# Optimization experiments

Hardware: AMD Instinct MI355X
Metric: run time of the kernel (lower is better)

Reference implementation:

```python
import jax, jax.numpy as jnp
import numpy as np
from jax import lax

P = 10  # patch_size


def _conv(x, w, b, pad):
    y = lax.conv_general_dilated(x, w, (1, 1), [(pad, pad), (pad, pad)],
                                 dimension_numbers=('NCHW', 'OIHW', 'NCHW'))
    return y + b[None, :, None, None]


def setup_inputs() -> dict:
    key = jax.random.key(0)
    ks = jax.random.split(key, 9)
    B, Cin, H, W = 8, 3, 320, 320
    classes = 2
    p2 = P * P
    s = 0.05
    return {
        'x': jax.random.normal(ks[0], (B, Cin, H, W), jnp.float32),
        'w_conv1': jax.random.normal(ks[1], (64, Cin, 7, 7), jnp.float32) * s,
        'b_conv1': jax.random.normal(ks[2], (64,), jnp.float32) * s,
        'w_conv2': jax.random.normal(ks[3], (classes, 64, 3, 3), jnp.float32) * s,
        'b_conv2': jax.random.normal(ks[4], (classes,), jnp.float32) * s,
        'w_fm': jax.random.normal(ks[5], (classes, Cin, 1, 1), jnp.float32) * s,
        'b_fm': jax.random.normal(ks[6], (classes,), jnp.float32) * s,
        'w_lin1': jax.random.normal(ks[7], (2 * p2, p2), jnp.float32) * s,  # torch Linear [out,in]
        'w_lin2': jax.random.normal(ks[8], (p2, 2 * p2), jnp.float32) * s,
    }


def reference(x, w_conv1, b_conv1, w_conv2, b_conv2, w_fm, b_fm, w_lin1, w_lin2):
    p = P
    ini = _conv(_conv(x, w_conv1, b_conv1, 3), w_conv2, b_conv2, 1)  # [B,classes,H,W]
    fea = _conv(x, w_fm, b_fm, 0) / 4.0                              # [B,classes,H,W]
    B, C, H, W = ini.shape
    L = (H // p) * (W // p)

    def unfold(t):  # non-overlapping patches: [B,C,H,W] -> [B,C,L,p*p]
        t = t.reshape(B, C, H // p, p, W // p, p)
        return t.transpose(0, 1, 2, 4, 3, 5).reshape(B, C, L, p * p)

    def trans(t):  # Linear(p2->2p2) -> Linear(2p2->p2) -> ReLU, per patch
        h = jnp.einsum('bclp,qp->bclq', t, w_lin1)
        return jax.nn.relu(jnp.einsum('bclq,pq->bclp', h, w_lin2))

    ui = trans(unfold(ini))   # [B,C,L,p2]
    uf = trans(unfold(fea))   # [B,C,L,p2]
    att = jnp.einsum('bclp,bcmp->bclm', ui, uf) / (p * p)  # [B,C,L,L]
    return att
```

## Files before the change

kernel.cpp:

```cpp
#include <hip/hip_runtime.h>

#define WS_M      0
#define WS_K      10000
#define WS_BETA   12646
#define WS_W9     12664
#define WS_BT     13150
#define WS_UIT    (16384 + 1638400)
#define WS_UFT    (16384 + 2*1638400)

typedef short bf16x8 __attribute__((ext_vector_type(8)));
typedef float f32x4  __attribute__((ext_vector_type(4)));

__device__ inline ushort f2bf(float f) {
    unsigned u = __float_as_uint(f);
    unsigned r = (u + 0x7fffu + ((u >> 16) & 1u)) >> 16;
    return (ushort)r;
}

__global__ __launch_bounds__(256) void k_prep(const float* __restrict__ wl1,
                                              const float* __restrict__ wl2,
                                              const float* __restrict__ wc1,
                                              const float* __restrict__ bc1,
                                              const float* __restrict__ wc2,
                                              const float* __restrict__ bc2,
                                              float* __restrict__ ws) {
    int blk = blockIdx.x;
    int t = threadIdx.x;
    if (blk < 40) {
        int idx = blk * 256 + t;
        if (idx < 10000) {
            int p = idx / 100, r = idx % 100;
            float s = 0.f;
            for (int q = 0; q < 200; ++q)
                s += wl2[p * 200 + q] * wl1[q * 100 + r];
            ws[WS_M + r * 100 + p] = s;
        }
        return;
    }
    __shared__ float swc1[9408];
    __shared__ float swc2[1152];
    __shared__ float sBeta[18];
    for (int i = t; i < 9408; i += 256) swc1[i] = wc1[i];
    for (int i = t; i < 1152; i += 256) swc2[i] = wc2[i];
    __syncthreads();
    if (blk < 43) {
        int base = (blk - 40) * 882;
        for (int ii = t; ii < 882; ii += 256) {
            int idx = base + ii;
            int v = idx % 7; int t1 = idx / 7;
            int u = t1 % 7;  int t2 = t1 / 7;
            int ci = t2 % 3; int t3 = t2 / 3;
            int b = t3 % 3;  int t4 = t3 / 3;
            int a = t4 % 3;  int c = t4 / 3;
            float s = 0.f;
            for (int c64 = 0; c64 < 64; ++c64)
                s += swc2[((c * 64 + c64) * 3 + a) * 3 + b] *
                     swc1[((c64 * 3 + ci) * 7 + u) * 7 + v];
            ws[WS_K + idx] = s;
        }
        if (blk == 40) {
            if (t < 18) {
                int b = t % 3; int a = (t / 3) % 3; int c = t / 9;
                float s = 0.f;
                for (int c64 = 0; c64 < 64; ++c64)
                    s += swc2[((c * 64 + c64) * 3 + a) * 3 + b] * bc1[c64];
                sBeta[t] = s; ws[WS_BETA + t] = s;
            }
            __syncthreads();
            if (t < 2) {
                float s = bc2[t];
                for (int j2 = 0; j2 < 9; ++j2) s += sBeta[t * 9 + j2];
                ws[WS_BT + t] = s;
            }
        }
    } else {
        int idx = (blk - 43) * 243 + t;
        if (t < 243) {
            int dx = idx % 9; int t1 = idx / 9;
            int dy = t1 % 9;  int t2 = t1 / 9;
            int ci = t2 % 3;  int c = t2 / 3;
            float s = 0.f;
            for (int a = 0; a < 3; ++a) {
                int u = dy - a; if (u < 0 || u > 6) continue;
                for (int b = 0; b < 3; ++b) {
                    int v = dx - b; if (v < 0 || v > 6) continue;
                    for (int c64 = 0; c64 < 64; ++c64)
                        s += swc2[((c * 64 + c64) * 3 + a) * 3 + b] *
                             swc1[((c64 * 3 + ci) * 7 + u) * 7 + v];
                }
            }
            ws[WS_W9 + idx] = s;
        }
    }
}

__global__ __launch_bounds__(256, 6) void k_fuse(const float* __restrict__ x,
                                                 const float* __restrict__ wfm,
                                                 const float* __restrict__ bfm,
                                                 const float* __restrict__ ws,
                                                 ushort* __restrict__ uiL,
                                                 ushort* __restrict__ ufL) {
    __shared__ float sx[3][28][36];
    __shared__ float sP[2][100][8];
    const int bx = blockIdx.x, by = blockIdx.y, b = blockIdx.z;
    const int t = threadIdx.x;
    const float* Mt   = ws + WS_M;
    const float* Kw   = ws + WS_K;
    const float* Beta = ws + WS_BETA;
    const float* W9   = ws + WS_W9;
    const float* Bt   = ws + WS_BT;
    const int gh0 = by * 20, gw0 = bx * 20;

    for (int idx = t; idx < 3 * 28 * 28; idx += 256) {
        int ci = idx / 784; int rem = idx - ci * 784;
        int rr = rem / 28, cc = rem - rr * 28;
        int gh = gh0 - 4 + rr, gw = gw0 - 4 + cc;
        float v = 0.f;
        if ((unsigned)gh < 320u && (unsigned)gw < 320u)
            v = x[(b * 3 + ci) * 102400 + gh * 320 + gw];
        sx[ci][rr][cc] = v;
    }
    __syncthreads();

    const int lh = t / 10, lw0 = (t % 10) * 2;
    if (t < 200) {
        float acc0[2], acc1[2];
        float bt0 = Bt[0], bt1 = Bt[1];
        acc0[0] = bt0; acc0[1] = bt0; acc1[0] = bt1; acc1[1] = bt1;
        #pragma unroll
        for (int ci = 0; ci < 3; ++ci) {
            #pragma unroll
            for (int dy = 0; dy < 9; ++dy) {
                const float* xr = &sx[ci][lh + dy][lw0];
                float2 y0 = *(const float2*)(xr);
                float2 y1 = *(const float2*)(xr + 2);
                float2 y2 = *(const float2*)(xr + 4);
                float2 y3 = *(const float2*)(xr + 6);
                float2 y4 = *(const float2*)(xr + 8);
                float xv[10] = {y0.x, y0.y, y1.x, y1.y, y2.x,
                                y2.y, y3.x, y3.y, y4.x, y4.y};
                #pragma unroll
                for (int dx = 0; dx < 9; ++dx) {
                    float w0t = W9[ci * 81 + dy * 9 + dx];
                    float w1t = W9[243 + ci * 81 + dy * 9 + dx];
                    acc0[0] += w0t * xv[dx];
                    acc0[1] += w0t * xv[dx + 1];
                    acc1[0] += w1t * xv[dx];
                    acc1[1] += w1t * xv[dx + 1];
                }
            }
        }
        #pragma unroll
        for (int j = 0; j < 2; ++j) {
            int lw = lw0 + j;
            int li = (lh / 10) * 2 + lw / 10;
            int r  = (lh % 10) * 10 + lw % 10;
            sP[0][r][li] = acc0[j];
            sP[1][r][li] = acc1[j];
        }
    }
    __syncthreads();

    bool edgeblk = (by == 0) | (by == 15) | (bx == 0) | (bx == 15);
    if (edgeblk) {
        for (int e = t; e < 400; e += 256) {
            int elh = e / 20, elw = e % 20;
            int h = gh0 + elh, w = gw0 + elw;
            if (h == 0 || h == 319 || w == 0 || w == 319) {
                float c0 = 0.f, c1 = 0.f;
                for (int a = 0; a < 3; ++a) {
                    int hh = h + a - 1;
                    for (int bb = 0; bb < 3; ++bb) {
                        int wwp = w + bb - 1;
                        bool invalid = ((unsigned)hh >= 320u) | ((unsigned)wwp >= 320u);
                        if (invalid) {
                            c0 += Beta[a * 3 + bb];
                            c1 += Beta[9 + a * 3 + bb];
                            for (int ci = 0; ci < 3; ++ci) {
                                const float* Kc = Kw + ((a * 3 + bb) * 3 + ci) * 49;
                                #pragma unroll
                                for (int u = 0; u < 7; ++u) {
                                    #pragma unroll
                                    for (int v = 0; v < 7; ++v) {
                                        float xv = sx[ci][elh + a + u][elw + bb + v];
                                        c0 += Kc[u * 7 + v] * xv;
                                        c1 += Kc[1323 + u * 7 + v] * xv;
                                    }
                                }
                            }
                        }
                    }
                }
                int li = (elh / 10) * 2 + elw / 10;
                int r  = (elh % 10) * 10 + elw % 10;
                sP[0][r][li] -= c0;
                sP[1][r][li] -= c1;
            }
        }
    }
    __syncthreads();

    auto trans = [&](ushort* outL) {
        if (t < 200) {
            int plane = (t >= 100) ? 1 : 0;
            int p = t - plane * 100;
            int bc = b * 2 + plane;
            float acc[4] = {0.f, 0.f, 0.f, 0.f};
            for (int r = 0; r < 100; ++r) {
                float m = Mt[r * 100 + p];
                f32x4 s = *(const f32x4*)&sP[plane][r][0];
                #pragma unroll
                for (int k = 0; k < 4; ++k) acc[k] += m * s[k];
            }
            #pragma unroll
            for (int k = 0; k < 4; ++k) {
                int l = (by * 2 + (k >> 1)) * 32 + bx * 2 + (k & 1);
                outL[((size_t)bc * 1024 + l) * 128 + p] = f2bf(fmaxf(acc[k], 0.f));
            }
        } else if (t < 256) {
            int task = t - 200;
            if (task < 56) {
                int plane = task / 28; int rem = task % 28;
                int k = rem / 7, q = rem % 7;
                int bc = b * 2 + plane;
                int l = (by * 2 + (k >> 1)) * 32 + bx * 2 + (k & 1);
                *(uint2*)&outL[((size_t)bc * 1024 + l) * 128 + 100 + q * 4] =
                    make_uint2(0u, 0u);
            }
        }
    };

    trans(uiL);
    __syncthreads();

    if (t < 200) {
        float wf00 = wfm[0], wf01 = wfm[1], wf02 = wfm[2];
        float wf10 = wfm[3], wf11 = wfm[4], wf12 = wfm[5];
        float bf0 = bfm[0], bf1 = bfm[1];
        #pragma unroll
        for (int j = 0; j < 2; ++j) {
            int lw = lw0 + j;
            float s0 = sx[0][4 + lh][4 + lw];
            float s1 = sx[1][4 + lh][4 + lw];
            float s2 = sx[2][4 + lh][4 + lw];
            float v0 = (bf0 + s0 * wf00 + s1 * wf01 + s2 * wf02) * 0.25f;
            float v1 = (bf1 + s0 * wf10 + s1 * wf11 + s2 * wf12) * 0.25f;
            int li = (lh / 10) * 2 + lw / 10;
            int r  = (lh % 10) * 10 + lw % 10;
            sP[0][r][li] = v0;
            sP[1][r][li] = v1;
        }
    }
    __syncthreads();

    trans(ufL);
}

__global__ __launch_bounds__(256) void k_att(const ushort* __restrict__ ui,
                                             const ushort* __restrict__ uf,
                                             float* __restrict__ out) {
    int bc   = blockIdx.z;
    int row0 = blockIdx.y * 128, col0 = blockIdx.x * 128;
    int wave = threadIdx.x >> 6, lane = threadIdx.x & 63;
    int r0 = row0 + (wave >> 1) * 64;
    int c0 = col0 + (wave & 1) * 64;
    int m = lane & 15, quad = lane >> 4;
    const ushort* ub = ui + (size_t)bc * 1024 * 128;
    const ushort* vb = uf + (size_t)bc * 1024 * 128;
    f32x4 acc[4][4];
    #pragma unroll
    for (int i = 0; i < 4; ++i)
        #pragma unroll
        for (int j = 0; j < 4; ++j)
            acc[i][j] = (f32x4){0.f, 0.f, 0.f, 0.f};
    #pragma unroll
    for (int k0 = 0; k0 < 128; k0 += 32) {
        bf16x8 af[4], bfr[4];
        #pragma unroll
        for (int i = 0; i < 4; ++i)
            af[i] = *(const bf16x8*)&ub[(size_t)(r0 + i * 16 + m) * 128 + k0 + quad * 8];
        #pragma unroll
        for (int j = 0; j < 4; ++j)
            bfr[j] = *(const bf16x8*)&vb[(size_t)(c0 + j * 16 + m) * 128 + k0 + quad * 8];
        #pragma unroll
        for (int i = 0; i < 4; ++i)
            #pragma unroll
            for (int j = 0; j < 4; ++j)
                acc[i][j] = __builtin_amdgcn_mfma_f32_16x16x32_bf16(af[i], bfr[j], acc[i][j], 0, 0, 0);
    }
    #pragma unroll
    for (int i = 0; i < 4; ++i) {
        #pragma unroll
        for (int r = 0; r < 4; ++r) {
            int row = r0 + i * 16 + quad * 4 + r;
            float* o = out + ((size_t)bc * 1024 + row) * 1024;
            #pragma unroll
            for (int j = 0; j < 4; ++j)
                o[c0 + j * 16 + m] = acc[i][j][r] * 0.01f;
        }
    }
}

extern "C" void kernel_launch(void* const* d_in, const int* in_sizes, int n_in,
                              void* d_out, int out_size, void* d_ws, size_t ws_size,
                              hipStream_t stream) {
    const float* x       = (const float*)d_in[0];
    const float* w_conv1 = (const float*)d_in[1];
    const float* b_conv1 = (const float*)d_in[2];
    const float* w_conv2 = (const float*)d_in[3];
    const float* b_conv2 = (const float*)d_in[4];
    const float* w_fm    = (const float*)d_in[5];
    const float* b_fm    = (const float*)d_in[6];
    const float* w_lin1  = (const float*)d_in[7];
    const float* w_lin2  = (const float*)d_in[8];
    float* out = (float*)d_out;
    float* ws  = (float*)d_ws;
    ushort* uiL = (ushort*)(ws + WS_UIT);
    ushort* ufL = (ushort*)(ws + WS_UFT);

    k_prep<<<45, 256, 0, stream>>>(w_lin1, w_lin2, w_conv1, b_conv1, w_conv2, b_conv2, ws);
    k_fuse<<<dim3(16, 16, 8), 256, 0, stream>>>(x, w_fm, b_fm, ws, uiL, ufL);
    k_att<<<dim3(8, 8, 16), 256, 0, stream>>>(uiL, ufL, out);
}
```

Measured before the change: 212.0 us.

## Stage patch outputs in shared memory for vector stores and shrink attention tiles

```diff
diff --git a/kernel.cpp b/kernel.cpp
--- a/kernel.cpp
+++ b/kernel.cpp
@@ -94,13 +94,17 @@
     }
 }
 
-__global__ __launch_bounds__(256, 6) void k_fuse(const float* __restrict__ x,
+__global__ __launch_bounds__(256, 8) void k_fuse(const float* __restrict__ x,
                                                  const float* __restrict__ wfm,
                                                  const float* __restrict__ bfm,
                                                  const float* __restrict__ ws,
                                                  ushort* __restrict__ uiL,
                                                  ushort* __restrict__ ufL) {
-    __shared__ float sx[3][28][36];
+    union alignas(16) SMemU {
+        float  sx[3][28][36];
+        ushort sOut[2][4][128];
+    };
+    __shared__ SMemU smu;
     __shared__ float sP[2][100][8];
     const int bx = blockIdx.x, by = blockIdx.y, b = blockIdx.z;
     const int t = threadIdx.x;
@@ -118,7 +122,7 @@
         float v = 0.f;
         if ((unsigned)gh < 320u && (unsigned)gw < 320u)
             v = x[(b * 3 + ci) * 102400 + gh * 320 + gw];
-        sx[ci][rr][cc] = v;
+        smu.sx[ci][rr][cc] = v;
     }
     __syncthreads();
 
@@ -131,7 +135,7 @@
         for (int ci = 0; ci < 3; ++ci) {
             #pragma unroll
             for (int dy = 0; dy < 9; ++dy) {
-                const float* xr = &sx[ci][lh + dy][lw0];
+                const float* xr = &smu.sx[ci][lh + dy][lw0];
                 float2 y0 = *(const float2*)(xr);
                 float2 y1 = *(const float2*)(xr + 2);
                 float2 y2 = *(const float2*)(xr + 4);
@@ -182,7 +186,7 @@
                                 for (int u = 0; u < 7; ++u) {
                                     #pragma unroll
                                     for (int v = 0; v < 7; ++v) {
-                                        float xv = sx[ci][elh + a + u][elw + bb + v];
+                                        float xv = smu.sx[ci][elh + a + u][elw + bb + v];
                                         c0 += Kc[u * 7 + v] * xv;
                                         c1 += Kc[1323 + u * 7 + v] * xv;
                                     }
@@ -200,12 +204,12 @@
     }
     __syncthreads();
 
-    auto trans = [&](ushort* outL) {
+    auto trans_compute = [&]() {
         if (t < 200) {
             int plane = (t >= 100) ? 1 : 0;
             int p = t - plane * 100;
-            int bc = b * 2 + plane;
             float acc[4] = {0.f, 0.f, 0.f, 0.f};
+            #pragma unroll 4
             for (int r = 0; r < 100; ++r) {
                 float m = Mt[r * 100 + p];
                 f32x4 s = *(const f32x4*)&sP[plane][r][0];
@@ -213,38 +217,47 @@
                 for (int k = 0; k < 4; ++k) acc[k] += m * s[k];
             }
             #pragma unroll
-            for (int k = 0; k < 4; ++k) {
-                int l = (by * 2 + (k >> 1)) * 32 + bx * 2 + (k & 1);
-                outL[((size_t)bc * 1024 + l) * 128 + p] = f2bf(fmaxf(acc[k], 0.f));
-            }
-        } else if (t < 256) {
+            for (int k = 0; k < 4; ++k)
+                smu.sOut[plane][k][p] = f2bf(fmaxf(acc[k], 0.f));
+        } else {
             int task = t - 200;
-            if (task < 56) {
-                int plane = task / 28; int rem = task % 28;
-                int k = rem / 7, q = rem % 7;
-                int bc = b * 2 + plane;
-                int l = (by * 2 + (k >> 1)) * 32 + bx * 2 + (k & 1);
-                *(uint2*)&outL[((size_t)bc * 1024 + l) * 128 + 100 + q * 4] =
-                    make_uint2(0u, 0u);
-            }
+            int plane = task / 28; int rem = task % 28;
+            int k = rem / 7, q = rem % 7;
+            *(uint2*)&smu.sOut[plane][k][100 + q * 4] = make_uint2(0u, 0u);
         }
     };
-
-    trans(uiL);
-    __syncthreads();
-
+    auto writeout = [&](ushort* outL) {
+        if (t < 128) {
+            int row = t >> 4;
+            int plane = row >> 2, k = row & 3;
+            int lane16 = t & 15;
+            int bc = b * 2 + plane;
+            int l = (by * 2 + (k >> 1)) * 32 + bx * 2 + (k & 1);
+            uint4 v = *(const uint4*)&smu.sOut[plane][k][lane16 * 8];
+            *(uint4*)&outL[((size_t)bc * 1024 + l) * 128 + lane16 * 8] = v;
+        }
+    };
+
+    trans_compute();
+    __syncthreads();
+    writeout(uiL);
     if (t < 200) {
         float wf00 = wfm[0], wf01 = wfm[1], wf02 = wfm[2];
         float wf10 = wfm[3], wf11 = wfm[4], wf12 = wfm[5];
         float bf0 = bfm[0], bf1 = bfm[1];
+        int gh = gh0 + lh, gwb = gw0 + lw0;
+        size_t base = (size_t)b * 3 * 102400 + gh * 320 + gwb;
+        float2 c0v = *(const float2*)&x[base];
+        float2 c1v = *(const float2*)&x[base + 102400];
+        float2 c2v = *(const float2*)&x[base + 204800];
+        float s0[2] = {c0v.x, c0v.y};
+        float s1[2] = {c1v.x, c1v.y};
+        float s2[2] = {c2v.x, c2v.y};
         #pragma unroll
         for (int j = 0; j < 2; ++j) {
+            float v0 = (bf0 + s0[j] * wf00 + s1[j] * wf01 + s2[j] * wf02) * 0.25f;
+            float v1 = (bf1 + s0[j] * wf10 + s1[j] * wf11 + s2[j] * wf12) * 0.25f;
             int lw = lw0 + j;
-            float s0 = sx[0][4 + lh][4 + lw];
-            float s1 = sx[1][4 + lh][4 + lw];
-            float s2 = sx[2][4 + lh][4 + lw];
-            float v0 = (bf0 + s0 * wf00 + s1 * wf01 + s2 * wf02) * 0.25f;
-            float v1 = (bf1 + s0 * wf10 + s1 * wf11 + s2 * wf12) * 0.25f;
             int li = (lh / 10) * 2 + lw / 10;
             int r  = (lh % 10) * 10 + lw % 10;
             sP[0][r][li] = v0;
@@ -253,43 +266,45 @@
     }
     __syncthreads();
 
-    trans(ufL);
+    trans_compute();
+    __syncthreads();
+    writeout(ufL);
 }
 
 __global__ __launch_bounds__(256) void k_att(const ushort* __restrict__ ui,
                                              const ushort* __restrict__ uf,
                                              float* __restrict__ out) {
     int bc   = blockIdx.z;
-    int row0 = blockIdx.y * 128, col0 = blockIdx.x * 128;
+    int row0 = blockIdx.y * 64, col0 = blockIdx.x * 128;
     int wave = threadIdx.x >> 6, lane = threadIdx.x & 63;
-    int r0 = row0 + (wave >> 1) * 64;
+    int r0 = row0 + (wave >> 1) * 32;
     int c0 = col0 + (wave & 1) * 64;
     int m = lane & 15, quad = lane >> 4;
     const ushort* ub = ui + (size_t)bc * 1024 * 128;
     const ushort* vb = uf + (size_t)bc * 1024 * 128;
-    f32x4 acc[4][4];
+    f32x4 acc[2][4];
     #pragma unroll
-    for (int i = 0; i < 4; ++i)
+    for (int i = 0; i < 2; ++i)
         #pragma unroll
         for (int j = 0; j < 4; ++j)
             acc[i][j] = (f32x4){0.f, 0.f, 0.f, 0.f};
     #pragma unroll
     for (int k0 = 0; k0 < 128; k0 += 32) {
-        bf16x8 af[4], bfr[4];
-        #pragma unroll
-        for (int i = 0; i < 4; ++i)
+        bf16x8 af[2], bfr[4];
+        #pragma unroll
+        for (int i = 0; i < 2; ++i)
             af[i] = *(const bf16x8*)&ub[(size_t)(r0 + i * 16 + m) * 128 + k0 + quad * 8];
         #pragma unroll
         for (int j = 0; j < 4; ++j)
             bfr[j] = *(const bf16x8*)&vb[(size_t)(c0 + j * 16 + m) * 128 + k0 + quad * 8];
         #pragma unroll
-        for (int i = 0; i < 4; ++i)
+        for (int i = 0; i < 2; ++i)
             #pragma unroll
             for (int j = 0; j < 4; ++j)
                 acc[i][j] = __builtin_amdgcn_mfma_f32_16x16x32_bf16(af[i], bfr[j], acc[i][j], 0, 0, 0);
     }
     #pragma unroll
-    for (int i = 0; i < 4; ++i) {
+    for (int i = 0; i < 2; ++i) {
         #pragma unroll
         for (int r = 0; r < 4; ++r) {
             int row = r0 + i * 16 + quad * 4 + r;
@@ -320,5 +335,5 @@
 
     k_prep<<<45, 256, 0, stream>>>(w_lin1, w_lin2, w_conv1, b_conv1, w_conv2, b_conv2, ws);
     k_fuse<<<dim3(16, 16, 8), 256, 0, stream>>>(x, w_fm, b_fm, ws, uiL, ufL);
-    k_att<<<dim3(8, 8, 16), 256, 0, stream>>>(uiL, ufL, out);
-}
+    k_att<<<dim3(8, 16, 16), 256, 0, stream>>>(uiL, ufL, out);
+}
```

Result: faster. 204.8 us (-3.4%).
